# Kernel optimization log

Measured on AMD Instinct MI355X. Metric: run time of the kernel, lower is better.

The kernel has to match this reference:

```python
import jax, jax.numpy as jnp
import numpy as np

WS = (4, 4, 4)  # window shape (wd, wh, ww)
EPS = 1e-5


def _layernorm(x, g, b):
    mu = jnp.mean(x, axis=-1, keepdims=True)
    var = jnp.mean(jnp.square(x - mu), axis=-1, keepdims=True)
    return (x - mu) * jax.lax.rsqrt(var + EPS) * g + b


def _partition(x, ws):
    # x: [B, D, H, W, C] -> [num_windows, wd*wh*ww, C]
    B, D, H, W, C = x.shape
    x = x.reshape(B, D // ws[0], ws[0], H // ws[1], ws[1], W // ws[2], ws[2], C)
    x = jnp.transpose(x, (0, 1, 3, 5, 2, 4, 6, 7))
    return x.reshape(-1, ws[0] * ws[1] * ws[2], C)


def _merge(win, shape, ws):
    B, D, H, W, C = shape
    x = win.reshape(B, D // ws[0], H // ws[1], W // ws[2], ws[0], ws[1], ws[2], C)
    x = jnp.transpose(x, (0, 1, 4, 2, 5, 3, 6, 7))
    return x.reshape(B, D, H, W, C)


def setup_inputs() -> dict:
    key = jax.random.key(0)
    ks = jax.random.split(key, 8)
    B, D, H, W, C = 2, 32, 64, 64, 96
    nh, kd = 4, 24
    s = 0.02
    return {
        "x": jax.random.normal(ks[0], (B, D, H, W, C), jnp.float32),
        "ln1_g": jnp.ones((C,), jnp.float32),
        "ln1_b": jnp.zeros((C,), jnp.float32),
        "wq": jax.random.normal(ks[1], (C, nh, kd), jnp.float32) * s,
        "bq": jnp.zeros((nh, kd), jnp.float32),
        "wk": jax.random.normal(ks[2], (C, nh, kd), jnp.float32) * s,
        "bk": jnp.zeros((nh, kd), jnp.float32),
        "wv": jax.random.normal(ks[3], (C, nh, kd), jnp.float32) * s,
        "bv": jnp.zeros((nh, kd), jnp.float32),
        "wo": jax.random.normal(ks[4], (nh, kd, C), jnp.float32) * s,
        "bo": jnp.zeros((C,), jnp.float32),
        "ln2_g": jnp.ones((C,), jnp.float32),
        "ln2_b": jnp.zeros((C,), jnp.float32),
        "w1": jax.random.normal(ks[5], (C, 4 * C), jnp.float32) * s,
        "b1": jnp.zeros((4 * C,), jnp.float32),
        "w2": jax.random.normal(ks[6], (4 * C, C), jnp.float32) * s,
        "b2": jnp.zeros((C,), jnp.float32),
    }


def reference(x, ln1_g, ln1_b, wq, bq, wk, bk, wv, bv, wo, bo,
              ln2_g, ln2_b, w1, b1, w2, b2):
    shape = x.shape  # [B, D, H, W, C]; dims chosen divisible by WS -> pad is a no-op
    kd = wq.shape[-1]
    shortcut = x
    h = _layernorm(x, ln1_g, ln1_b)
    win = _partition(h, WS)  # [n, L, C], L = 64
    # Keras MultiHeadAttention (inference, dropout off)
    q = jnp.einsum("nlc,chd->nlhd", win, wq) + bq
    k = jnp.einsum("nlc,chd->nlhd", win, wk) + bk
    v = jnp.einsum("nlc,chd->nlhd", win, wv) + bv
    scores = jnp.einsum("nlhd,nmhd->nhlm", q, k) / jnp.sqrt(jnp.float32(kd))
    attn = jax.nn.softmax(scores, axis=-1)
    o = jnp.einsum("nhlm,nmhd->nlhd", attn, v)
    out = jnp.einsum("nlhd,hdc->nlc", o, wo) + bo
    x = shortcut + _merge(out, shape, WS)
    shortcut = x
    h = _layernorm(x, ln2_g, ln2_b)
    h = jax.nn.gelu(h @ w1 + b1, approximate=False)  # TF keras 'gelu' is exact
    h = h @ w2 + b2
    return shortcut + h
```

## Files before the change

kernel.cpp:

```cpp
#include <hip/hip_runtime.h>
#include <hip/hip_bf16.h>

typedef __attribute__((ext_vector_type(8))) short short8;
typedef __attribute__((ext_vector_type(4))) short short4b;
typedef __attribute__((ext_vector_type(4))) float f32x4;
typedef unsigned short ushort_t;

#define NTOK 262144

__device__ __forceinline__ ushort_t f2bf(float f){
  __hip_bfloat16 h = __float2bfloat16(f);
  return *reinterpret_cast<ushort_t*>(&h);
}
__device__ __forceinline__ float bf2f(ushort_t u){
  union { unsigned int i; float f; } v; v.i = ((unsigned int)u) << 16; return v.f;
}
__device__ __forceinline__ float fast_rcp(float x){
  float r; asm("v_rcp_f32 %0, %1" : "=v"(r) : "v"(x)); return r;
}
__device__ __forceinline__ float gelu_f(float x){
  float e = __expf(-1.702f * x);
  return x * fast_rcp(1.0f + e);
}
__device__ __forceinline__ void bar_lds(){
  asm volatile("s_waitcnt lgkmcnt(0)" ::: "memory");
  __builtin_amdgcn_s_barrier();
  __builtin_amdgcn_sched_barrier(0);
}
__device__ __forceinline__ void bar_cnt3(){
  asm volatile("s_waitcnt vmcnt(3) lgkmcnt(0)" ::: "memory");
  __builtin_amdgcn_s_barrier();
  __builtin_amdgcn_sched_barrier(0);
}
__device__ __forceinline__ void bar_cnt5(){
  asm volatile("s_waitcnt vmcnt(5) lgkmcnt(0)" ::: "memory");
  __builtin_amdgcn_s_barrier();
  __builtin_amdgcn_sched_barrier(0);
}
__device__ __forceinline__ void bar_cnt0(){
  asm volatile("s_waitcnt vmcnt(0) lgkmcnt(0)" ::: "memory");
  __builtin_amdgcn_s_barrier();
  __builtin_amdgcn_sched_barrier(0);
}
__device__ __forceinline__ void gl_lds16(const ushort_t* g, ushort_t* l){
  __builtin_amdgcn_global_load_lds(
      (const __attribute__((address_space(1))) void*)g,
      (__attribute__((address_space(3))) void*)l, 16, 0, 0);
}

__device__ __forceinline__ void stage_half3(const ushort_t* __restrict__ src,
                                            ushort_t* __restrict__ dst, int tid)
{
  #pragma unroll
  for (int it = 0; it < 3; ++it) {
    int u = tid + it * 256;
    const ushort_t* sp = src + (size_t)((u < 576) ? u : 0) * 8;
    gl_lds16(sp, dst + (size_t)(u & ~63) * 8);
  }
}

__device__ __forceinline__ void stage_wp(const ushort_t* __restrict__ src,
                                         int src_stride, ushort_t* __restrict__ dst, int tid)
{
  #pragma unroll
  for (int it = 0; it < 5; ++it) {
    int u = tid + it * 256;
    int row = u / 13, c16 = u % 13;
    const ushort_t* sp = src + row * src_stride + ((c16 >= 12) ? 0 : c16 * 8);
    gl_lds16(sp, dst + (size_t)(u & ~63) * 8);
  }
}

__global__ __launch_bounds__(256) void prep_kernel(
    const float* __restrict__ wq, const float* __restrict__ wk, const float* __restrict__ wv,
    const float* __restrict__ wo, const float* __restrict__ w1, const float* __restrict__ w2,
    const float* __restrict__ bq, const float* __restrict__ bk, const float* __restrict__ bv,
    ushort_t* __restrict__ Wqkv, ushort_t* __restrict__ Wo,
    ushort_t* __restrict__ W1, ushort_t* __restrict__ W2, float* __restrict__ biasq)
{
  const float qs = 0.20412414523193150818f;
  int i = blockIdx.x * 256 + threadIdx.x;
  if (i < 27648) {
    int j = i / 96, c = i % 96;
    int s = j / 96, rem = j % 96;
    const float* src = (s == 0) ? wq : (s == 1) ? wk : wv;
    float val = src[c * 96 + rem];
    if (s == 0) val *= qs;
    Wqkv[j * 96 + c] = f2bf(val);
  } else if (i < 36864) {
    int ii = i - 27648;
    int c = ii / 96, hd = ii % 96;
    Wo[ii] = f2bf(wo[hd * 96 + c]);
  } else if (i < 73728) {
    int ii = i - 36864;
    int j = ii / 96, c = ii % 96;
    W1[ii] = f2bf(w1[c * 384 + j]);
  } else if (i < 110592) {
    int ii = i - 73728;
    int c = ii / 384, j = ii % 384;
    W2[ii] = f2bf(w2[j * 96 + c]);
  } else if (i < 110880) {
    int j = i - 110592;
    int s = j / 96, rem = j % 96;
    const float* src = (s == 0) ? bq : (s == 1) ? bk : bv;
    float val = src[rem];
    if (s == 0) val *= qs;
    biasq[j] = val;
  }
}

__global__ __launch_bounds__(256, 2) void fat_kernel(
    const float* __restrict__ x, const float* __restrict__ g, const float* __restrict__ b,
    const ushort_t* __restrict__ Wqkv, const float* __restrict__ biasq,
    const ushort_t* __restrict__ Wo, const float* __restrict__ bo,
    ushort_t* __restrict__ x2b)
{
  __shared__ ushort_t regionA[18432];
  __shared__ ushort_t Vt[4][32][72];
  __shared__ ushort_t WsH[2][6144];
  ushort_t (*hbt)[104]   = reinterpret_cast<ushort_t(*)[104]>(regionA);
  ushort_t (*QK)[200]    = reinterpret_cast<ushort_t(*)[200]>(regionA);
  ushort_t (*Pb)[64][72] = reinterpret_cast<ushort_t(*)[64][72]>(regionA);
  ushort_t (*O_lds)[104] = reinterpret_cast<ushort_t(*)[104]>(regionA);

  int tid = threadIdx.x;
  int n = blockIdx.x;
  int wq_ = n & 15, hq = (n >> 4) & 15, rest = n >> 8;
  int dq = rest & 7, bb_ = rest >> 3;
  int base = bb_ * 131072 + dq * 16384 + hq * 256 + wq_ * 4;
  #define TOK(s) (base + ((s) >> 4) * 4096 + (((s) >> 2) & 3) * 64 + ((s) & 3))

  stage_half3(Wqkv, WsH[0], tid);
  stage_half3(Wqkv + 4608, WsH[1], tid);

  {
    int s = tid >> 2, qr = tid & 3;
    const float* xp = x + (size_t)TOK(s) * 96 + qr * 24;
    f32x4 v[6];
    float sm = 0.f, sq = 0.f;
    #pragma unroll
    for (int i = 0; i < 6; i++) {
      v[i] = *reinterpret_cast<const f32x4*>(xp + i * 4);
      #pragma unroll
      for (int j = 0; j < 4; j++) { sm += v[i][j]; sq += v[i][j] * v[i][j]; }
    }
    sm += __shfl_xor(sm, 1); sq += __shfl_xor(sq, 1);
    sm += __shfl_xor(sm, 2); sq += __shfl_xor(sq, 2);
    float mean = sm * (1.0f / 96.0f);
    float var  = sq * (1.0f / 96.0f) - mean * mean;
    float rstd = rsqrtf(var + 1e-5f);
    #pragma unroll
    for (int i8 = 0; i8 < 3; i8++) {
      short8 pk;
      #pragma unroll
      for (int j = 0; j < 8; j++) {
        int c = qr * 24 + i8 * 8 + j;
        pk[j] = (short)f2bf((v[(i8 * 8 + j) >> 2][(i8 * 8 + j) & 3] - mean) * rstd * g[c] + b[c]);
      }
      *reinterpret_cast<short8*>(&hbt[s][qr * 24 + i8 * 8]) = pk;
    }
  }

  int w = tid >> 6, lane = tid & 63, g16 = lane >> 4, l15 = lane & 15;
  short8 af[3];
  #pragma unroll
  for (int ks = 0; ks < 3; ks++)
    af[ks] = *reinterpret_cast<const short8*>(&hbt[w * 16 + l15][ks * 32 + g16 * 8]);
  __builtin_amdgcn_sched_barrier(0);

  int hidx = 0;
  for (int grp = 0; grp < 3; ++grp) {
    for (int half = 0; half < 2; ++half) {
      const ushort_t* buf = WsH[hidx & 1];
      bar_cnt3();
      f32x4 acc[3];
      #pragma unroll
      for (int jj = 0; jj < 3; jj++) acc[jj] = (f32x4){0.f, 0.f, 0.f, 0.f};
      __builtin_amdgcn_s_setprio(1);
      #pragma unroll
      for (int jj = 0; jj < 3; jj++)
        #pragma unroll
        for (int ks = 0; ks < 3; ks++) {
          short8 wfr = *reinterpret_cast<const short8*>(&buf[(jj * 16 + l15) * 96 + ks * 32 + g16 * 8]);
          acc[jj] = __builtin_amdgcn_mfma_f32_16x16x32_bf16(wfr, af[ks], acc[jj], 0, 0, 0);
        }
      __builtin_amdgcn_s_setprio(0);
      bar_lds();
      {
        const ushort_t* s2 = (hidx + 2 < 6) ? Wqkv + (size_t)(hidx + 2) * 4608
                                            : Wo + (size_t)(hidx - 4) * 4608;
        stage_half3(s2, WsH[hidx & 1], tid);
      }
      if (grp < 2) {
        #pragma unroll
        for (int jj = 0; jj < 3; jj++) {
          int c0 = grp * 96 + (half * 3 + jj) * 16 + g16 * 4;
          f32x4 bb4 = *reinterpret_cast<const f32x4*>(&biasq[c0]);
          unsigned lo = (unsigned)f2bf(acc[jj][0] + bb4[0]) | ((unsigned)f2bf(acc[jj][1] + bb4[1]) << 16);
          unsigned hi = (unsigned)f2bf(acc[jj][2] + bb4[2]) | ((unsigned)f2bf(acc[jj][3] + bb4[3]) << 16);
          uint2 pk; pk.x = lo; pk.y = hi;
          *reinterpret_cast<uint2*>(&QK[w * 16 + l15][c0]) = pk;
        }
      } else {
        #pragma unroll
        for (int jj = 0; jj < 3; jj++) {
          int c0 = (half * 3 + jj) * 16 + g16 * 4;
          f32x4 bb4 = *reinterpret_cast<const f32x4*>(&biasq[192 + c0]);
          #pragma unroll
          for (int r = 0; r < 4; r++) {
            int vcol = c0 + r;
            int h2 = vcol / 24, d2 = vcol - h2 * 24;
            Vt[h2][d2][w * 16 + l15] = f2bf(acc[jj][r] + bb4[r]);
          }
        }
      }
      hidx++;
    }
  }
  bar_lds();

  int h = w;
  short8 kf[4], qf[4];
  const short8 z8 = {0, 0, 0, 0, 0, 0, 0, 0};
  #pragma unroll
  for (int i = 0; i < 4; i++) {
    qf[i] = (g16 < 3) ? *(const short8*)&QK[i * 16 + l15][h * 24 + g16 * 8]      : z8;
    kf[i] = (g16 < 3) ? *(const short8*)&QK[i * 16 + l15][96 + h * 24 + g16 * 8] : z8;
  }
  f32x4 st[4][4];
  __builtin_amdgcn_s_setprio(1);
  #pragma unroll
  for (int tm = 0; tm < 4; tm++)
    #pragma unroll
    for (int tn = 0; tn < 4; tn++)
      st[tm][tn] = __builtin_amdgcn_mfma_f32_16x16x32_bf16(kf[tm], qf[tn],
                    (f32x4){0.f, 0.f, 0.f, 0.f}, 0, 0, 0);
  __builtin_amdgcn_s_setprio(0);
  bar_lds();

  #pragma unroll
  for (int tn = 0; tn < 4; tn++) {
    float m = st[0][tn][0];
    #pragma unroll
    for (int tm = 0; tm < 4; tm++)
      #pragma unroll
      for (int r = 0; r < 4; r++) m = fmaxf(m, st[tm][tn][r]);
    m = fmaxf(m, __shfl_xor(m, 16));
    m = fmaxf(m, __shfl_xor(m, 32));
    float sum = 0.f;
    #pragma unroll
    for (int tm = 0; tm < 4; tm++)
      #pragma unroll
      for (int r = 0; r < 4; r++) {
        float e = __expf(st[tm][tn][r] - m);
        st[tm][tn][r] = e;
        sum += e;
      }
    sum += __shfl_xor(sum, 16);
    sum += __shfl_xor(sum, 32);
    float inv = fast_rcp(sum);
    int q = tn * 16 + l15;
    #pragma unroll
    for (int tm = 0; tm < 4; tm++) {
      unsigned lo = (unsigned)f2bf(st[tm][tn][0] * inv) | ((unsigned)f2bf(st[tm][tn][1] * inv) << 16);
      unsigned hi = (unsigned)f2bf(st[tm][tn][2] * inv) | ((unsigned)f2bf(st[tm][tn][3] * inv) << 16);
      uint2 pk; pk.x = lo; pk.y = hi;
      *(uint2*)&Pb[h][q][tm * 16 + g16 * 4] = pk;
    }
  }

  f32x4 oacc[4][2];
  #pragma unroll
  for (int qt = 0; qt < 4; qt++)
    #pragma unroll
    for (int dt = 0; dt < 2; dt++) oacc[qt][dt] = (f32x4){0.f, 0.f, 0.f, 0.f};
  __builtin_amdgcn_s_setprio(1);
  #pragma unroll
  for (int ks = 0; ks < 2; ks++) {
    short8 vb[2];
    #pragma unroll
    for (int dt = 0; dt < 2; dt++)
      vb[dt] = *(const short8*)&Vt[h][dt * 16 + l15][ks * 32 + g16 * 8];
    #pragma unroll
    for (int qt = 0; qt < 4; qt++) {
      short8 pa = *(const short8*)&Pb[h][qt * 16 + l15][ks * 32 + g16 * 8];
      #pragma unroll
      for (int dt = 0; dt < 2; dt++)
        oacc[qt][dt] = __builtin_amdgcn_mfma_f32_16x16x32_bf16(pa, vb[dt], oacc[qt][dt], 0, 0, 0);
    }
  }
  __builtin_amdgcn_s_setprio(0);

  bar_lds();
  #pragma unroll
  for (int qt = 0; qt < 4; qt++)
    #pragma unroll
    for (int dt = 0; dt < 2; dt++) {
      int d = dt * 16 + l15;
      if (d < 24) {
        #pragma unroll
        for (int r = 0; r < 4; r++)
          O_lds[qt * 16 + g16 * 4 + r][h * 24 + d] = f2bf(oacc[qt][dt][r]);
      }
    }
  bar_cnt0();

  f32x4 pacc[6];
  #pragma unroll
  for (int nt = 0; nt < 6; nt++) pacc[nt] = (f32x4){0.f, 0.f, 0.f, 0.f};
  __builtin_amdgcn_s_setprio(1);
  #pragma unroll
  for (int ks = 0; ks < 3; ks++) {
    short8 pa = *(const short8*)&O_lds[w * 16 + l15][ks * 32 + g16 * 8];
    #pragma unroll
    for (int nt = 0; nt < 6; nt++) {
      const ushort_t* buf = WsH[(nt < 3) ? 0 : 1];
      short8 wb = *reinterpret_cast<const short8*>(&buf[((nt % 3) * 16 + l15) * 96 + ks * 32 + g16 * 8]);
      pacc[nt] = __builtin_amdgcn_mfma_f32_16x16x32_bf16(wb, pa, pacc[nt], 0, 0, 0);
    }
  }
  __builtin_amdgcn_s_setprio(0);
  {
    size_t t = (size_t)TOK(w * 16 + l15);
    #pragma unroll
    for (int nt = 0; nt < 6; nt++) {
      int c0 = nt * 16 + g16 * 4;
      f32x4 bo4 = *reinterpret_cast<const f32x4*>(&bo[c0]);
      f32x4 xr  = *reinterpret_cast<const f32x4*>(&x[t * 96 + c0]);
      float v0 = pacc[nt][0] + bo4[0] + xr[0];
      float v1 = pacc[nt][1] + bo4[1] + xr[1];
      float v2 = pacc[nt][2] + bo4[2] + xr[2];
      float v3 = pacc[nt][3] + bo4[3] + xr[3];
      unsigned lo = (unsigned)f2bf(v0) | ((unsigned)f2bf(v1) << 16);
      unsigned hi = (unsigned)f2bf(v2) | ((unsigned)f2bf(v3) << 16);
      uint2 pk; pk.x = lo; pk.y = hi;
      *reinterpret_cast<uint2*>(&x2b[t * 96 + c0]) = pk;
    }
  }
  #undef TOK
}

__device__ __forceinline__ void ln_to_lds_b(const ushort_t* __restrict__ xrow_base,
    const float* __restrict__ gg, const float* __restrict__ bb,
    ushort_t (*hbt)[104], int tid)
{
  int row = tid >> 1, half = tid & 1;
  const ushort_t* xp = xrow_base + (size_t)row * 96 + half * 48;
  short8 vv[6];
  #pragma unroll
  for (int i = 0; i < 6; i++) vv[i] = *reinterpret_cast<const short8*>(xp + i * 8);
  float v[48];
  float s = 0.f, sq = 0.f;
  #pragma unroll
  for (int i = 0; i < 6; i++)
    #pragma unroll
    for (int j = 0; j < 8; j++) {
      float f = bf2f((ushort_t)vv[i][j]);
      v[i * 8 + j] = f; s += f; sq += f * f;
    }
  s  += __shfl_xor(s, 1);
  sq += __shfl_xor(sq, 1);
  float mean = s * (1.0f / 96.0f);
  float var  = sq * (1.0f / 96.0f) - mean * mean;
  float rstd = rsqrtf(var + 1e-5f);
  #pragma unroll
  for (int i8 = 0; i8 < 6; i8++) {
    short8 pk;
    #pragma unroll
    for (int j = 0; j < 8; j++) {
      int c = half * 48 + i8 * 8 + j;
      pk[j] = (short)f2bf((v[i8 * 8 + j] - mean) * rstd * gg[c] + bb[c]);
    }
    *reinterpret_cast<short8*>(&hbt[row][half * 48 + i8 * 8]) = pk;
  }
}

__global__ __launch_bounds__(256, 2) void mlp2_kernel(
    const ushort_t* __restrict__ x2b, const float* __restrict__ g, const float* __restrict__ b,
    const ushort_t* __restrict__ W1t, const float* __restrict__ b1,
    const ushort_t* __restrict__ W2t, const float* __restrict__ b2,
    float* __restrict__ out)
{
  __shared__ ushort_t smem[128][104];
  __shared__ ushort_t WsA[10240];
  __shared__ ushort_t WsB[10240];
  __shared__ float bias1[384];
  __shared__ float bias2[96];
  int tid = threadIdx.x;
  size_t r0 = (size_t)blockIdx.x * 128;

  stage_wp(W1t, 96, WsA, tid);
  stage_wp(W2t, 384, WsB, tid);
  bias1[tid] = b1[tid];
  if (tid < 128) bias1[256 + tid] = b1[256 + tid];
  if (tid < 96)  bias2[tid] = b2[tid];
  ln_to_lds_b(x2b + r0 * 96, g, b, smem, tid);

  int w = tid >> 6, lane = tid & 63, g16 = lane >> 4, l15 = lane & 15;
  short8 af[2][3];
  #pragma unroll
  for (int mi = 0; mi < 2; mi++)
    #pragma unroll
    for (int ks = 0; ks < 3; ks++)
      af[mi][ks] = *reinterpret_cast<const short8*>(&smem[w * 32 + mi * 16 + l15][ks * 32 + g16 * 8]);
  __builtin_amdgcn_sched_barrier(0);

  f32x4 oacc[6][2];
  #pragma unroll
  for (int nt = 0; nt < 6; nt++) { oacc[nt][0] = (f32x4){0.f,0.f,0.f,0.f}; oacc[nt][1] = (f32x4){0.f,0.f,0.f,0.f}; }

  for (int cc = 0; cc < 4; ++cc) {
    bar_cnt5();
    f32x4 acc[6][2];
    #pragma unroll
    for (int nt = 0; nt < 6; nt++) { acc[nt][0] = (f32x4){0.f,0.f,0.f,0.f}; acc[nt][1] = (f32x4){0.f,0.f,0.f,0.f}; }
    __builtin_amdgcn_s_setprio(1);
    #pragma unroll
    for (int nt = 0; nt < 6; nt++)
      #pragma unroll
      for (int ks = 0; ks < 3; ks++) {
        short8 wfr = *reinterpret_cast<const short8*>(&WsA[(nt * 16 + l15) * 104 + ks * 32 + g16 * 8]);
        acc[nt][0] = __builtin_amdgcn_mfma_f32_16x16x32_bf16(wfr, af[0][ks], acc[nt][0], 0, 0, 0);
        acc[nt][1] = __builtin_amdgcn_mfma_f32_16x16x32_bf16(wfr, af[1][ks], acc[nt][1], 0, 0, 0);
      }
    __builtin_amdgcn_s_setprio(0);
    #pragma unroll
    for (int nt = 0; nt < 6; nt++) {
      f32x4 bb4 = *reinterpret_cast<const f32x4*>(&bias1[cc * 96 + nt * 16 + g16 * 4]);
      #pragma unroll
      for (int mi = 0; mi < 2; mi++) {
        float g0 = gelu_f(acc[nt][mi][0] + bb4[0]);
        float g1 = gelu_f(acc[nt][mi][1] + bb4[1]);
        float g2 = gelu_f(acc[nt][mi][2] + bb4[2]);
        float g3 = gelu_f(acc[nt][mi][3] + bb4[3]);
        unsigned lo = (unsigned)f2bf(g0) | ((unsigned)f2bf(g1) << 16);
        unsigned hi = (unsigned)f2bf(g2) | ((unsigned)f2bf(g3) << 16);
        uint2 pk; pk.x = lo; pk.y = hi;
        *reinterpret_cast<uint2*>(&smem[w * 32 + mi * 16 + l15][nt * 16 + g16 * 4]) = pk;
      }
    }
    short8 a2[2][3];
    #pragma unroll
    for (int mi = 0; mi < 2; mi++)
      #pragma unroll
      for (int ks = 0; ks < 3; ks++)
        a2[mi][ks] = *reinterpret_cast<const short8*>(&smem[w * 32 + mi * 16 + l15][ks * 32 + g16 * 8]);
    bar_lds();
    if (cc < 3) stage_wp(W1t + (cc + 1) * 9216, 96, WsA, tid);
    if (cc < 3) bar_cnt5(); else bar_cnt0();
    __builtin_amdgcn_s_setprio(1);
    #pragma unroll
    for (int nt = 0; nt < 6; nt++)
      #pragma unroll
      for (int ks = 0; ks < 3; ks++) {
        short8 wfr = *reinterpret_cast<const short8*>(&WsB[(nt * 16 + l15) * 104 + ks * 32 + g16 * 8]);
        oacc[nt][0] = __builtin_amdgcn_mfma_f32_16x16x32_bf16(wfr, a2[0][ks], oacc[nt][0], 0, 0, 0);
        oacc[nt][1] = __builtin_amdgcn_mfma_f32_16x16x32_bf16(wfr, a2[1][ks], oacc[nt][1], 0, 0, 0);
      }
    __builtin_amdgcn_s_setprio(0);
    if (cc < 3) {
      bar_lds();
      stage_wp(W2t + (cc + 1) * 96, 384, WsB, tid);
    }
  }

  #pragma unroll
  for (int nt = 0; nt < 6; nt++) {
    int c0 = nt * 16 + g16 * 4;
    f32x4 bb4 = *reinterpret_cast<const f32x4*>(&bias2[c0]);
    #pragma unroll
    for (int mi = 0; mi < 2; mi++) {
      size_t row = r0 + w * 32 + mi * 16 + l15;
      short4b rr = *reinterpret_cast<const short4b*>(&x2b[row * 96 + c0]);
      f32x4 o;
      #pragma unroll
      for (int r = 0; r < 4; r++) o[r] = oacc[nt][mi][r] + bb4[r] + bf2f((ushort_t)rr[r]);
      *reinterpret_cast<f32x4*>(&out[row * 96 + c0]) = o;
    }
  }
}

extern "C" void kernel_launch(void* const* d_in, const int* in_sizes, int n_in,
                              void* d_out, int out_size, void* d_ws, size_t ws_size,
                              hipStream_t stream)
{
  (void)in_sizes; (void)n_in; (void)out_size; (void)ws_size;
  const float* x    = (const float*)d_in[0];
  const float* ln1g = (const float*)d_in[1];
  const float* ln1b = (const float*)d_in[2];
  const float* wq   = (const float*)d_in[3];
  const float* bq   = (const float*)d_in[4];
  const float* wk   = (const float*)d_in[5];
  const float* bk   = (const float*)d_in[6];
  const float* wv   = (const float*)d_in[7];
  const float* bv   = (const float*)d_in[8];
  const float* wo   = (const float*)d_in[9];
  const float* bo   = (const float*)d_in[10];
  const float* ln2g = (const float*)d_in[11];
  const float* ln2b = (const float*)d_in[12];
  const float* w1   = (const float*)d_in[13];
  const float* b1   = (const float*)d_in[14];
  const float* w2   = (const float*)d_in[15];
  const float* b2   = (const float*)d_in[16];

  char* ws = (char*)d_ws;
  ushort_t* x2b  = (ushort_t*)(ws);
  char* wsw      = ws + 50331648;
  ushort_t* Wqkv = (ushort_t*)(wsw);
  ushort_t* Wo   = (ushort_t*)(wsw + 55296);
  ushort_t* W1   = (ushort_t*)(wsw + 55296 + 18432);
  ushort_t* W2   = (ushort_t*)(wsw + 55296 + 18432 + 73728);
  float*    biasq= (float*)   (wsw + 55296 + 18432 + 73728 + 73728);

  prep_kernel<<<434, 256, 0, stream>>>(wq, wk, wv, wo, w1, w2, bq, bk, bv,
                                       Wqkv, Wo, W1, W2, biasq);
  fat_kernel<<<4096, 256, 0, stream>>>(x, ln1g, ln1b, Wqkv, biasq, Wo, bo, x2b);
  mlp2_kernel<<<NTOK / 128, 256, 0, stream>>>(x2b, ln2g, ln2b, W1, b1, W2, b2, (float*)d_out);
}
```

Baseline: 189.7 us.

## Fuse MLP block into windowed attention kernel, eliminating bf16 intermediate round-trip

Merges the separate MLP kernel into the attention kernel. Each block now computes LN2, the W1 GEMM with GELU, and the W2 GEMM for its 64 window tokens, reusing the double-buffered weight staging ring with W2 repacked into chunked transposed halves. This removes the 50MB bf16 intermediate write and read and one kernel launch. In exchange, each block now reads all MLP weights for only 64 tokens instead of 128, and the larger LDS footprint may cut occupancy.

```diff
diff --git a/kernel.cpp b/kernel.cpp
--- a/kernel.cpp
+++ b/kernel.cpp
@@ -32,11 +32,6 @@
   __builtin_amdgcn_s_barrier();
   __builtin_amdgcn_sched_barrier(0);
 }
-__device__ __forceinline__ void bar_cnt5(){
-  asm volatile("s_waitcnt vmcnt(5) lgkmcnt(0)" ::: "memory");
-  __builtin_amdgcn_s_barrier();
-  __builtin_amdgcn_sched_barrier(0);
-}
 __device__ __forceinline__ void bar_cnt0(){
   asm volatile("s_waitcnt vmcnt(0) lgkmcnt(0)" ::: "memory");
   __builtin_amdgcn_s_barrier();
@@ -59,16 +54,14 @@
   }
 }
 
-__device__ __forceinline__ void stage_wp(const ushort_t* __restrict__ src,
-                                         int src_stride, ushort_t* __restrict__ dst, int tid)
+__device__ __forceinline__ const ushort_t* stage_src(int hidx,
+    const ushort_t* Wqkv, const ushort_t* Wo, const ushort_t* W1t, const ushort_t* W2c)
 {
-  #pragma unroll
-  for (int it = 0; it < 5; ++it) {
-    int u = tid + it * 256;
-    int row = u / 13, c16 = u % 13;
-    const ushort_t* sp = src + row * src_stride + ((c16 >= 12) ? 0 : c16 * 8);
-    gl_lds16(sp, dst + (size_t)(u & ~63) * 8);
-  }
+  if (hidx < 6) return Wqkv + (size_t)hidx * 4608;
+  if (hidx < 8) return Wo + (size_t)(hidx - 6) * 4608;
+  int m = hidx - 8, cc = m >> 2, p = m & 3;
+  const ushort_t* base = (p < 2) ? W1t : W2c;
+  return base + (size_t)cc * 9216 + (size_t)(p & 1) * 4608;
 }
 
 __global__ __launch_bounds__(256) void prep_kernel(
@@ -76,7 +69,7 @@
     const float* __restrict__ wo, const float* __restrict__ w1, const float* __restrict__ w2,
     const float* __restrict__ bq, const float* __restrict__ bk, const float* __restrict__ bv,
     ushort_t* __restrict__ Wqkv, ushort_t* __restrict__ Wo,
-    ushort_t* __restrict__ W1, ushort_t* __restrict__ W2, float* __restrict__ biasq)
+    ushort_t* __restrict__ W1, ushort_t* __restrict__ W2c, float* __restrict__ biasq)
 {
   const float qs = 0.20412414523193150818f;
   int i = blockIdx.x * 256 + threadIdx.x;
@@ -97,8 +90,9 @@
     W1[ii] = f2bf(w1[c * 384 + j]);
   } else if (i < 110592) {
     int ii = i - 73728;
-    int c = ii / 384, j = ii % 384;
-    W2[ii] = f2bf(w2[j * 96 + c]);
+    int cc = ii / 9216, rem = ii % 9216;
+    int j = rem / 96, kk = rem % 96;
+    W2c[ii] = f2bf(w2[(size_t)(cc * 96 + kk) * 96 + j]);
   } else if (i < 110880) {
     int j = i - 110592;
     int s = j / 96, rem = j % 96;
@@ -109,19 +103,25 @@
   }
 }
 
-__global__ __launch_bounds__(256, 2) void fat_kernel(
+__global__ __launch_bounds__(256, 2) void fat2_kernel(
     const float* __restrict__ x, const float* __restrict__ g, const float* __restrict__ b,
     const ushort_t* __restrict__ Wqkv, const float* __restrict__ biasq,
     const ushort_t* __restrict__ Wo, const float* __restrict__ bo,
-    ushort_t* __restrict__ x2b)
+    const float* __restrict__ ln2g, const float* __restrict__ ln2b,
+    const ushort_t* __restrict__ W1t, const float* __restrict__ b1,
+    const ushort_t* __restrict__ W2c, const float* __restrict__ b2,
+    float* __restrict__ outp)
 {
-  __shared__ ushort_t regionA[18432];
+  __shared__ ushort_t regionA[19456];
   __shared__ ushort_t Vt[4][32][72];
   __shared__ ushort_t WsH[2][6144];
   ushort_t (*hbt)[104]   = reinterpret_cast<ushort_t(*)[104]>(regionA);
   ushort_t (*QK)[200]    = reinterpret_cast<ushort_t(*)[200]>(regionA);
   ushort_t (*Pb)[64][72] = reinterpret_cast<ushort_t(*)[64][72]>(regionA);
   ushort_t (*O_lds)[104] = reinterpret_cast<ushort_t(*)[104]>(regionA);
+  ushort_t* h_ln = regionA;
+  ushort_t* mid  = regionA + 6656;
+  ushort_t* x2L  = regionA + 13312;
 
   int tid = threadIdx.x;
   int n = blockIdx.x;
@@ -168,53 +168,46 @@
     af[ks] = *reinterpret_cast<const short8*>(&hbt[w * 16 + l15][ks * 32 + g16 * 8]);
   __builtin_amdgcn_sched_barrier(0);
 
-  int hidx = 0;
-  for (int grp = 0; grp < 3; ++grp) {
-    for (int half = 0; half < 2; ++half) {
-      const ushort_t* buf = WsH[hidx & 1];
-      bar_cnt3();
-      f32x4 acc[3];
-      #pragma unroll
-      for (int jj = 0; jj < 3; jj++) acc[jj] = (f32x4){0.f, 0.f, 0.f, 0.f};
-      __builtin_amdgcn_s_setprio(1);
-      #pragma unroll
-      for (int jj = 0; jj < 3; jj++)
+  for (int hidx = 0; hidx < 6; ++hidx) {
+    const ushort_t* buf = WsH[hidx & 1];
+    bar_cnt3();
+    f32x4 acc[3];
+    #pragma unroll
+    for (int jj = 0; jj < 3; jj++) acc[jj] = (f32x4){0.f, 0.f, 0.f, 0.f};
+    __builtin_amdgcn_s_setprio(1);
+    #pragma unroll
+    for (int jj = 0; jj < 3; jj++)
+      #pragma unroll
+      for (int ks = 0; ks < 3; ks++) {
+        short8 wfr = *reinterpret_cast<const short8*>(&buf[(jj * 16 + l15) * 96 + ks * 32 + g16 * 8]);
+        acc[jj] = __builtin_amdgcn_mfma_f32_16x16x32_bf16(wfr, af[ks], acc[jj], 0, 0, 0);
+      }
+    __builtin_amdgcn_s_setprio(0);
+    bar_lds();
+    stage_half3(stage_src(hidx + 2, Wqkv, Wo, W1t, W2c), WsH[hidx & 1], tid);
+    int grp = hidx >> 1, half = hidx & 1;
+    if (grp < 2) {
+      #pragma unroll
+      for (int jj = 0; jj < 3; jj++) {
+        int c0 = grp * 96 + (half * 3 + jj) * 16 + g16 * 4;
+        f32x4 bb4 = *reinterpret_cast<const f32x4*>(&biasq[c0]);
+        unsigned lo = (unsigned)f2bf(acc[jj][0] + bb4[0]) | ((unsigned)f2bf(acc[jj][1] + bb4[1]) << 16);
+        unsigned hi = (unsigned)f2bf(acc[jj][2] + bb4[2]) | ((unsigned)f2bf(acc[jj][3] + bb4[3]) << 16);
+        uint2 pk; pk.x = lo; pk.y = hi;
+        *reinterpret_cast<uint2*>(&QK[w * 16 + l15][c0]) = pk;
+      }
+    } else {
+      #pragma unroll
+      for (int jj = 0; jj < 3; jj++) {
+        int c0 = (half * 3 + jj) * 16 + g16 * 4;
+        f32x4 bb4 = *reinterpret_cast<const f32x4*>(&biasq[192 + c0]);
         #pragma unroll
-        for (int ks = 0; ks < 3; ks++) {
-          short8 wfr = *reinterpret_cast<const short8*>(&buf[(jj * 16 + l15) * 96 + ks * 32 + g16 * 8]);
-          acc[jj] = __builtin_amdgcn_mfma_f32_16x16x32_bf16(wfr, af[ks], acc[jj], 0, 0, 0);
+        for (int r = 0; r < 4; r++) {
+          int vcol = c0 + r;
+          int h2 = vcol / 24, d2 = vcol - h2 * 24;
+          Vt[h2][d2][w * 16 + l15] = f2bf(acc[jj][r] + bb4[r]);
         }
-      __builtin_amdgcn_s_setprio(0);
-      bar_lds();
-      {
-        const ushort_t* s2 = (hidx + 2 < 6) ? Wqkv + (size_t)(hidx + 2) * 4608
-                                            : Wo + (size_t)(hidx - 4) * 4608;
-        stage_half3(s2, WsH[hidx & 1], tid);
-      }
-      if (grp < 2) {
-        #pragma unroll
-        for (int jj = 0; jj < 3; jj++) {
-          int c0 = grp * 96 + (half * 3 + jj) * 16 + g16 * 4;
-          f32x4 bb4 = *reinterpret_cast<const f32x4*>(&biasq[c0]);
-          unsigned lo = (unsigned)f2bf(acc[jj][0] + bb4[0]) | ((unsigned)f2bf(acc[jj][1] + bb4[1]) << 16);
-          unsigned hi = (unsigned)f2bf(acc[jj][2] + bb4[2]) | ((unsigned)f2bf(acc[jj][3] + bb4[3]) << 16);
-          uint2 pk; pk.x = lo; pk.y = hi;
-          *reinterpret_cast<uint2*>(&QK[w * 16 + l15][c0]) = pk;
-        }
-      } else {
-        #pragma unroll
-        for (int jj = 0; jj < 3; jj++) {
-          int c0 = (half * 3 + jj) * 16 + g16 * 4;
-          f32x4 bb4 = *reinterpret_cast<const f32x4*>(&biasq[192 + c0]);
-          #pragma unroll
-          for (int r = 0; r < 4; r++) {
-            int vcol = c0 + r;
-            int h2 = vcol / 24, d2 = vcol - h2 * 24;
-            Vt[h2][d2][w * 16 + l15] = f2bf(acc[jj][r] + bb4[r]);
-          }
-        }
-      }
-      hidx++;
+      }
     }
   }
   bar_lds();
@@ -269,11 +262,11 @@
     }
   }
 
-  f32x4 oacc[4][2];
+  f32x4 oatt[4][2];
   #pragma unroll
   for (int qt = 0; qt < 4; qt++)
     #pragma unroll
-    for (int dt = 0; dt < 2; dt++) oacc[qt][dt] = (f32x4){0.f, 0.f, 0.f, 0.f};
+    for (int dt = 0; dt < 2; dt++) oatt[qt][dt] = (f32x4){0.f, 0.f, 0.f, 0.f};
   __builtin_amdgcn_s_setprio(1);
   #pragma unroll
   for (int ks = 0; ks < 2; ks++) {
@@ -286,7 +279,7 @@
       short8 pa = *(const short8*)&Pb[h][qt * 16 + l15][ks * 32 + g16 * 8];
       #pragma unroll
       for (int dt = 0; dt < 2; dt++)
-        oacc[qt][dt] = __builtin_amdgcn_mfma_f32_16x16x32_bf16(pa, vb[dt], oacc[qt][dt], 0, 0, 0);
+        oatt[qt][dt] = __builtin_amdgcn_mfma_f32_16x16x32_bf16(pa, vb[dt], oatt[qt][dt], 0, 0, 0);
     }
   }
   __builtin_amdgcn_s_setprio(0);
@@ -300,7 +293,7 @@
       if (d < 24) {
         #pragma unroll
         for (int r = 0; r < 4; r++)
-          O_lds[qt * 16 + g16 * 4 + r][h * 24 + d] = f2bf(oacc[qt][dt][r]);
+          O_lds[qt * 16 + g16 * 4 + r][h * 24 + d] = f2bf(oatt[qt][dt][r]);
       }
     }
   bar_cnt0();
@@ -320,164 +313,127 @@
     }
   }
   __builtin_amdgcn_s_setprio(0);
+  bar_lds();
+  stage_half3(stage_src(8, Wqkv, Wo, W1t, W2c), WsH[0], tid);
+  stage_half3(stage_src(9, Wqkv, Wo, W1t, W2c), WsH[1], tid);
+
+  size_t t = (size_t)TOK(w * 16 + l15);
+  int rowoff = (w * 16 + l15);
   {
-    size_t t = (size_t)TOK(w * 16 + l15);
+    float xv[24];
+    float sm = 0.f, sq = 0.f;
     #pragma unroll
     for (int nt = 0; nt < 6; nt++) {
       int c0 = nt * 16 + g16 * 4;
       f32x4 bo4 = *reinterpret_cast<const f32x4*>(&bo[c0]);
       f32x4 xr  = *reinterpret_cast<const f32x4*>(&x[t * 96 + c0]);
-      float v0 = pacc[nt][0] + bo4[0] + xr[0];
-      float v1 = pacc[nt][1] + bo4[1] + xr[1];
-      float v2 = pacc[nt][2] + bo4[2] + xr[2];
-      float v3 = pacc[nt][3] + bo4[3] + xr[3];
-      unsigned lo = (unsigned)f2bf(v0) | ((unsigned)f2bf(v1) << 16);
-      unsigned hi = (unsigned)f2bf(v2) | ((unsigned)f2bf(v3) << 16);
-      uint2 pk; pk.x = lo; pk.y = hi;
-      *reinterpret_cast<uint2*>(&x2b[t * 96 + c0]) = pk;
-    }
-  }
-  #undef TOK
-}
-
-__device__ __forceinline__ void ln_to_lds_b(const ushort_t* __restrict__ xrow_base,
-    const float* __restrict__ gg, const float* __restrict__ bb,
-    ushort_t (*hbt)[104], int tid)
-{
-  int row = tid >> 1, half = tid & 1;
-  const ushort_t* xp = xrow_base + (size_t)row * 96 + half * 48;
-  short8 vv[6];
-  #pragma unroll
-  for (int i = 0; i < 6; i++) vv[i] = *reinterpret_cast<const short8*>(xp + i * 8);
-  float v[48];
-  float s = 0.f, sq = 0.f;
-  #pragma unroll
-  for (int i = 0; i < 6; i++)
-    #pragma unroll
-    for (int j = 0; j < 8; j++) {
-      float f = bf2f((ushort_t)vv[i][j]);
-      v[i * 8 + j] = f; s += f; sq += f * f;
-    }
-  s  += __shfl_xor(s, 1);
-  sq += __shfl_xor(sq, 1);
-  float mean = s * (1.0f / 96.0f);
-  float var  = sq * (1.0f / 96.0f) - mean * mean;
-  float rstd = rsqrtf(var + 1e-5f);
-  #pragma unroll
-  for (int i8 = 0; i8 < 6; i8++) {
-    short8 pk;
-    #pragma unroll
-    for (int j = 0; j < 8; j++) {
-      int c = half * 48 + i8 * 8 + j;
-      pk[j] = (short)f2bf((v[i8 * 8 + j] - mean) * rstd * gg[c] + bb[c]);
-    }
-    *reinterpret_cast<short8*>(&hbt[row][half * 48 + i8 * 8]) = pk;
-  }
-}
-
-__global__ __launch_bounds__(256, 2) void mlp2_kernel(
-    const ushort_t* __restrict__ x2b, const float* __restrict__ g, const float* __restrict__ b,
-    const ushort_t* __restrict__ W1t, const float* __restrict__ b1,
-    const ushort_t* __restrict__ W2t, const float* __restrict__ b2,
-    float* __restrict__ out)
-{
-  __shared__ ushort_t smem[128][104];
-  __shared__ ushort_t WsA[10240];
-  __shared__ ushort_t WsB[10240];
-  __shared__ float bias1[384];
-  __shared__ float bias2[96];
-  int tid = threadIdx.x;
-  size_t r0 = (size_t)blockIdx.x * 128;
-
-  stage_wp(W1t, 96, WsA, tid);
-  stage_wp(W2t, 384, WsB, tid);
-  bias1[tid] = b1[tid];
-  if (tid < 128) bias1[256 + tid] = b1[256 + tid];
-  if (tid < 96)  bias2[tid] = b2[tid];
-  ln_to_lds_b(x2b + r0 * 96, g, b, smem, tid);
-
-  int w = tid >> 6, lane = tid & 63, g16 = lane >> 4, l15 = lane & 15;
-  short8 af[2][3];
-  #pragma unroll
-  for (int mi = 0; mi < 2; mi++)
-    #pragma unroll
-    for (int ks = 0; ks < 3; ks++)
-      af[mi][ks] = *reinterpret_cast<const short8*>(&smem[w * 32 + mi * 16 + l15][ks * 32 + g16 * 8]);
+      #pragma unroll
+      for (int r = 0; r < 4; r++) {
+        float v = pacc[nt][r] + bo4[r] + xr[r];
+        xv[nt * 4 + r] = v; sm += v; sq += v * v;
+      }
+    }
+    sm += __shfl_xor(sm, 16); sq += __shfl_xor(sq, 16);
+    sm += __shfl_xor(sm, 32); sq += __shfl_xor(sq, 32);
+    float mean = sm * (1.0f / 96.0f);
+    float var  = sq * (1.0f / 96.0f) - mean * mean;
+    float rstd = rsqrtf(var + 1e-5f);
+    #pragma unroll
+    for (int nt = 0; nt < 6; nt++) {
+      int c0 = nt * 16 + g16 * 4;
+      f32x4 g4 = *reinterpret_cast<const f32x4*>(&ln2g[c0]);
+      f32x4 b4 = *reinterpret_cast<const f32x4*>(&ln2b[c0]);
+      unsigned hlo, hhi, xlo, xhi;
+      float h0 = (xv[nt*4+0] - mean) * rstd * g4[0] + b4[0];
+      float h1 = (xv[nt*4+1] - mean) * rstd * g4[1] + b4[1];
+      float h2v = (xv[nt*4+2] - mean) * rstd * g4[2] + b4[2];
+      float h3 = (xv[nt*4+3] - mean) * rstd * g4[3] + b4[3];
+      hlo = (unsigned)f2bf(h0) | ((unsigned)f2bf(h1) << 16);
+      hhi = (unsigned)f2bf(h2v) | ((unsigned)f2bf(h3) << 16);
+      xlo = (unsigned)f2bf(xv[nt*4+0]) | ((unsigned)f2bf(xv[nt*4+1]) << 16);
+      xhi = (unsigned)f2bf(xv[nt*4+2]) | ((unsigned)f2bf(xv[nt*4+3]) << 16);
+      uint2 ph; ph.x = hlo; ph.y = hhi;
+      uint2 px; px.x = xlo; px.y = xhi;
+      *reinterpret_cast<uint2*>(&h_ln[rowoff * 104 + c0]) = ph;
+      *reinterpret_cast<uint2*>(&x2L[rowoff * 96 + c0]) = px;
+    }
+  }
+  short8 hf[3];
+  #pragma unroll
+  for (int ks = 0; ks < 3; ks++)
+    hf[ks] = *reinterpret_cast<const short8*>(&h_ln[rowoff * 104 + ks * 32 + g16 * 8]);
   __builtin_amdgcn_sched_barrier(0);
 
-  f32x4 oacc[6][2];
-  #pragma unroll
-  for (int nt = 0; nt < 6; nt++) { oacc[nt][0] = (f32x4){0.f,0.f,0.f,0.f}; oacc[nt][1] = (f32x4){0.f,0.f,0.f,0.f}; }
-
-  for (int cc = 0; cc < 4; ++cc) {
-    bar_cnt5();
-    f32x4 acc[6][2];
-    #pragma unroll
-    for (int nt = 0; nt < 6; nt++) { acc[nt][0] = (f32x4){0.f,0.f,0.f,0.f}; acc[nt][1] = (f32x4){0.f,0.f,0.f,0.f}; }
-    __builtin_amdgcn_s_setprio(1);
-    #pragma unroll
-    for (int nt = 0; nt < 6; nt++)
-      #pragma unroll
-      for (int ks = 0; ks < 3; ks++) {
-        short8 wfr = *reinterpret_cast<const short8*>(&WsA[(nt * 16 + l15) * 104 + ks * 32 + g16 * 8]);
-        acc[nt][0] = __builtin_amdgcn_mfma_f32_16x16x32_bf16(wfr, af[0][ks], acc[nt][0], 0, 0, 0);
-        acc[nt][1] = __builtin_amdgcn_mfma_f32_16x16x32_bf16(wfr, af[1][ks], acc[nt][1], 0, 0, 0);
-      }
-    __builtin_amdgcn_s_setprio(0);
-    #pragma unroll
-    for (int nt = 0; nt < 6; nt++) {
-      f32x4 bb4 = *reinterpret_cast<const f32x4*>(&bias1[cc * 96 + nt * 16 + g16 * 4]);
-      #pragma unroll
-      for (int mi = 0; mi < 2; mi++) {
-        float g0 = gelu_f(acc[nt][mi][0] + bb4[0]);
-        float g1 = gelu_f(acc[nt][mi][1] + bb4[1]);
-        float g2 = gelu_f(acc[nt][mi][2] + bb4[2]);
-        float g3 = gelu_f(acc[nt][mi][3] + bb4[3]);
+  f32x4 oacc[6];
+  #pragma unroll
+  for (int nt = 0; nt < 6; nt++) oacc[nt] = (f32x4){0.f, 0.f, 0.f, 0.f};
+  short8 mf[3];
+  for (int m = 0; m < 16; ++m) {
+    int cc = m >> 2, p = m & 3;
+    const ushort_t* buf = WsH[m & 1];
+    if (m == 15) bar_cnt0(); else bar_cnt3();
+    if (p < 2) {
+      f32x4 accM[3];
+      #pragma unroll
+      for (int jj = 0; jj < 3; jj++) accM[jj] = (f32x4){0.f, 0.f, 0.f, 0.f};
+      __builtin_amdgcn_s_setprio(1);
+      #pragma unroll
+      for (int jj = 0; jj < 3; jj++)
+        #pragma unroll
+        for (int ks = 0; ks < 3; ks++) {
+          short8 wfr = *reinterpret_cast<const short8*>(&buf[(jj * 16 + l15) * 96 + ks * 32 + g16 * 8]);
+          accM[jj] = __builtin_amdgcn_mfma_f32_16x16x32_bf16(wfr, hf[ks], accM[jj], 0, 0, 0);
+        }
+      __builtin_amdgcn_s_setprio(0);
+      bar_lds();
+      if (m + 2 <= 15) stage_half3(stage_src(10 + m, Wqkv, Wo, W1t, W2c), WsH[m & 1], tid);
+      #pragma unroll
+      for (int jj = 0; jj < 3; jj++) {
+        int lc = (p * 3 + jj) * 16 + g16 * 4;
+        f32x4 bb4 = *reinterpret_cast<const f32x4*>(&b1[cc * 96 + lc]);
+        float g0 = gelu_f(accM[jj][0] + bb4[0]);
+        float g1 = gelu_f(accM[jj][1] + bb4[1]);
+        float g2v = gelu_f(accM[jj][2] + bb4[2]);
+        float g3 = gelu_f(accM[jj][3] + bb4[3]);
         unsigned lo = (unsigned)f2bf(g0) | ((unsigned)f2bf(g1) << 16);
-        unsigned hi = (unsigned)f2bf(g2) | ((unsigned)f2bf(g3) << 16);
+        unsigned hi = (unsigned)f2bf(g2v) | ((unsigned)f2bf(g3) << 16);
         uint2 pk; pk.x = lo; pk.y = hi;
-        *reinterpret_cast<uint2*>(&smem[w * 32 + mi * 16 + l15][nt * 16 + g16 * 4]) = pk;
-      }
-    }
-    short8 a2[2][3];
-    #pragma unroll
-    for (int mi = 0; mi < 2; mi++)
-      #pragma unroll
-      for (int ks = 0; ks < 3; ks++)
-        a2[mi][ks] = *reinterpret_cast<const short8*>(&smem[w * 32 + mi * 16 + l15][ks * 32 + g16 * 8]);
-    bar_lds();
-    if (cc < 3) stage_wp(W1t + (cc + 1) * 9216, 96, WsA, tid);
-    if (cc < 3) bar_cnt5(); else bar_cnt0();
-    __builtin_amdgcn_s_setprio(1);
-    #pragma unroll
-    for (int nt = 0; nt < 6; nt++)
-      #pragma unroll
-      for (int ks = 0; ks < 3; ks++) {
-        short8 wfr = *reinterpret_cast<const short8*>(&WsB[(nt * 16 + l15) * 104 + ks * 32 + g16 * 8]);
-        oacc[nt][0] = __builtin_amdgcn_mfma_f32_16x16x32_bf16(wfr, a2[0][ks], oacc[nt][0], 0, 0, 0);
-        oacc[nt][1] = __builtin_amdgcn_mfma_f32_16x16x32_bf16(wfr, a2[1][ks], oacc[nt][1], 0, 0, 0);
-      }
-    __builtin_amdgcn_s_setprio(0);
-    if (cc < 3) {
-      bar_lds();
-      stage_wp(W2t + (cc + 1) * 96, 384, WsB, tid);
+        *reinterpret_cast<uint2*>(&mid[rowoff * 104 + lc]) = pk;
+      }
+      if (p == 1) {
+        #pragma unroll
+        for (int ks = 0; ks < 3; ks++)
+          mf[ks] = *reinterpret_cast<const short8*>(&mid[rowoff * 104 + ks * 32 + g16 * 8]);
+      }
+    } else {
+      int jb = (p - 2) * 3;
+      __builtin_amdgcn_s_setprio(1);
+      #pragma unroll
+      for (int jj = 0; jj < 3; jj++)
+        #pragma unroll
+        for (int ks = 0; ks < 3; ks++) {
+          short8 wfr = *reinterpret_cast<const short8*>(&buf[(jj * 16 + l15) * 96 + ks * 32 + g16 * 8]);
+          oacc[jb + jj] = __builtin_amdgcn_mfma_f32_16x16x32_bf16(wfr, mf[ks], oacc[jb + jj], 0, 0, 0);
+        }
+      __builtin_amdgcn_s_setprio(0);
+      if (m < 15) {
+        bar_lds();
+        if (m + 2 <= 15) stage_half3(stage_src(10 + m, Wqkv, Wo, W1t, W2c), WsH[m & 1], tid);
+      }
     }
   }
 
   #pragma unroll
   for (int nt = 0; nt < 6; nt++) {
     int c0 = nt * 16 + g16 * 4;
-    f32x4 bb4 = *reinterpret_cast<const f32x4*>(&bias2[c0]);
-    #pragma unroll
-    for (int mi = 0; mi < 2; mi++) {
-      size_t row = r0 + w * 32 + mi * 16 + l15;
-      short4b rr = *reinterpret_cast<const short4b*>(&x2b[row * 96 + c0]);
-      f32x4 o;
-      #pragma unroll
-      for (int r = 0; r < 4; r++) o[r] = oacc[nt][mi][r] + bb4[r] + bf2f((ushort_t)rr[r]);
-      *reinterpret_cast<f32x4*>(&out[row * 96 + c0]) = o;
-    }
-  }
+    f32x4 b24 = *reinterpret_cast<const f32x4*>(&b2[c0]);
+    short4b xr2 = *reinterpret_cast<const short4b*>(&x2L[rowoff * 96 + c0]);
+    f32x4 o;
+    #pragma unroll
+    for (int r = 0; r < 4; r++) o[r] = oacc[nt][r] + b24[r] + bf2f((ushort_t)xr2[r]);
+    *reinterpret_cast<f32x4*>(&outp[t * 96 + c0]) = o;
+  }
+  #undef TOK
 }
 
 extern "C" void kernel_launch(void* const* d_in, const int* in_sizes, int n_in,
@@ -504,16 +460,14 @@
   const float* b2   = (const float*)d_in[16];
 
   char* ws = (char*)d_ws;
-  ushort_t* x2b  = (ushort_t*)(ws);
-  char* wsw      = ws + 50331648;
-  ushort_t* Wqkv = (ushort_t*)(wsw);
-  ushort_t* Wo   = (ushort_t*)(wsw + 55296);
-  ushort_t* W1   = (ushort_t*)(wsw + 55296 + 18432);
-  ushort_t* W2   = (ushort_t*)(wsw + 55296 + 18432 + 73728);
-  float*    biasq= (float*)   (wsw + 55296 + 18432 + 73728 + 73728);
+  ushort_t* Wqkv = (ushort_t*)(ws);
+  ushort_t* Wo   = (ushort_t*)(ws + 55296);
+  ushort_t* W1   = (ushort_t*)(ws + 55296 + 18432);
+  ushort_t* W2c  = (ushort_t*)(ws + 55296 + 18432 + 73728);
+  float*    biasq= (float*)   (ws + 55296 + 18432 + 73728 + 73728);
 
   prep_kernel<<<434, 256, 0, stream>>>(wq, wk, wv, wo, w1, w2, bq, bk, bv,
-                                       Wqkv, Wo, W1, W2, biasq);
-  fat_kernel<<<4096, 256, 0, stream>>>(x, ln1g, ln1b, Wqkv, biasq, Wo, bo, x2b);
-  mlp2_kernel<<<NTOK / 128, 256, 0, stream>>>(x2b, ln2g, ln2b, W1, b1, W2, b2, (float*)d_out);
-}
+                                       Wqkv, Wo, W1, W2c, biasq);
+  fat2_kernel<<<4096, 256, 0, stream>>>(x, ln1g, ln1b, Wqkv, biasq, Wo, bo,
+                                        ln2g, ln2b, W1, b1, W2c, b2, (float*)d_out);
+}
```

Result: slower. 282.7 us (+49.0%).

## Shrink attention kernel LDS to single weight buffer for three blocks per CU

Applied to the files above, without the earlier changes.

Merges the attention kernel's shared arrays into one flat buffer and drops double-buffering of weight halves, loading each 4608-element weight slice into a single padded buffer with full waits. This cuts LDS per block so three blocks can reside per CU (launch bounds raised from 2 to 3). The softmax probability tile moves to an XOR-swizzled layout to avoid bank conflicts, the weight rows are padded to 104, and both kernels remap block IDs in groups of 8, likely to spread adjacent blocks across XCDs. The cost is losing prefetch overlap: every weight stage now waits with vmcnt(0) before its MFMAs.

```diff
diff --git a/kernel.cpp b/kernel.cpp
--- a/kernel.cpp
+++ b/kernel.cpp
@@ -27,11 +27,6 @@
   __builtin_amdgcn_s_barrier();
   __builtin_amdgcn_sched_barrier(0);
 }
-__device__ __forceinline__ void bar_cnt3(){
-  asm volatile("s_waitcnt vmcnt(3) lgkmcnt(0)" ::: "memory");
-  __builtin_amdgcn_s_barrier();
-  __builtin_amdgcn_sched_barrier(0);
-}
 __device__ __forceinline__ void bar_cnt5(){
   asm volatile("s_waitcnt vmcnt(5) lgkmcnt(0)" ::: "memory");
   __builtin_amdgcn_s_barrier();
@@ -48,14 +43,17 @@
       (__attribute__((address_space(3))) void*)l, 16, 0, 0);
 }
 
-__device__ __forceinline__ void stage_half3(const ushort_t* __restrict__ src,
-                                            ushort_t* __restrict__ dst, int tid)
+__device__ __forceinline__ void stage624(const ushort_t* __restrict__ src,
+                                         ushort_t* __restrict__ dst, int tid)
 {
   #pragma unroll
   for (int it = 0; it < 3; ++it) {
     int u = tid + it * 256;
-    const ushort_t* sp = src + (size_t)((u < 576) ? u : 0) * 8;
-    gl_lds16(sp, dst + (size_t)(u & ~63) * 8);
+    if (u < 624) {
+      int row = u / 13, c16 = u % 13;
+      const ushort_t* sp = src + row * 96 + ((c16 == 12) ? 0 : c16 * 8);
+      gl_lds16(sp, dst + (size_t)(u & ~63) * 8);
+    }
   }
 }
 
@@ -109,29 +107,24 @@
   }
 }
 
-__global__ __launch_bounds__(256, 2) void fat_kernel(
+__global__ __launch_bounds__(256, 3) void fat_kernel(
     const float* __restrict__ x, const float* __restrict__ g, const float* __restrict__ b,
     const ushort_t* __restrict__ Wqkv, const float* __restrict__ biasq,
     const ushort_t* __restrict__ Wo, const float* __restrict__ bo,
     ushort_t* __restrict__ x2b)
 {
-  __shared__ ushort_t regionA[18432];
-  __shared__ ushort_t Vt[4][32][72];
-  __shared__ ushort_t WsH[2][6144];
-  ushort_t (*hbt)[104]   = reinterpret_cast<ushort_t(*)[104]>(regionA);
-  ushort_t (*QK)[200]    = reinterpret_cast<ushort_t(*)[200]>(regionA);
-  ushort_t (*Pb)[64][72] = reinterpret_cast<ushort_t(*)[64][72]>(regionA);
-  ushort_t (*O_lds)[104] = reinterpret_cast<ushort_t(*)[104]>(regionA);
+  __shared__ ushort_t SM[27136];
+  const int WS_OFF = 12800, VT_OFF = 17920;
 
   int tid = threadIdx.x;
-  int n = blockIdx.x;
+  int bid = blockIdx.x;
+  int n = (bid & 7) * 512 + (bid >> 3);
   int wq_ = n & 15, hq = (n >> 4) & 15, rest = n >> 8;
   int dq = rest & 7, bb_ = rest >> 3;
   int base = bb_ * 131072 + dq * 16384 + hq * 256 + wq_ * 4;
   #define TOK(s) (base + ((s) >> 4) * 4096 + (((s) >> 2) & 3) * 64 + ((s) & 3))
 
-  stage_half3(Wqkv, WsH[0], tid);
-  stage_half3(Wqkv + 4608, WsH[1], tid);
+  stage624(Wqkv, SM + WS_OFF, tid);
 
   {
     int s = tid >> 2, qr = tid & 3;
@@ -157,7 +150,7 @@
         int c = qr * 24 + i8 * 8 + j;
         pk[j] = (short)f2bf((v[(i8 * 8 + j) >> 2][(i8 * 8 + j) & 3] - mean) * rstd * g[c] + b[c]);
       }
-      *reinterpret_cast<short8*>(&hbt[s][qr * 24 + i8 * 8]) = pk;
+      *reinterpret_cast<short8*>(&SM[s * 104 + qr * 24 + i8 * 8]) = pk;
     }
   }
 
@@ -165,56 +158,49 @@
   short8 af[3];
   #pragma unroll
   for (int ks = 0; ks < 3; ks++)
-    af[ks] = *reinterpret_cast<const short8*>(&hbt[w * 16 + l15][ks * 32 + g16 * 8]);
-  __builtin_amdgcn_sched_barrier(0);
-
-  int hidx = 0;
-  for (int grp = 0; grp < 3; ++grp) {
-    for (int half = 0; half < 2; ++half) {
-      const ushort_t* buf = WsH[hidx & 1];
-      bar_cnt3();
-      f32x4 acc[3];
-      #pragma unroll
-      for (int jj = 0; jj < 3; jj++) acc[jj] = (f32x4){0.f, 0.f, 0.f, 0.f};
-      __builtin_amdgcn_s_setprio(1);
-      #pragma unroll
-      for (int jj = 0; jj < 3; jj++)
+    af[ks] = *reinterpret_cast<const short8*>(&SM[(w * 16 + l15) * 104 + ks * 32 + g16 * 8]);
+  bar_lds();
+
+  for (int hidx = 0; hidx < 6; ++hidx) {
+    const ushort_t* buf = SM + WS_OFF;
+    bar_cnt0();
+    f32x4 acc[3];
+    #pragma unroll
+    for (int jj = 0; jj < 3; jj++) acc[jj] = (f32x4){0.f, 0.f, 0.f, 0.f};
+    __builtin_amdgcn_s_setprio(1);
+    #pragma unroll
+    for (int jj = 0; jj < 3; jj++)
+      #pragma unroll
+      for (int ks = 0; ks < 3; ks++) {
+        short8 wfr = *reinterpret_cast<const short8*>(&buf[(jj * 16 + l15) * 104 + ks * 32 + g16 * 8]);
+        acc[jj] = __builtin_amdgcn_mfma_f32_16x16x32_bf16(wfr, af[ks], acc[jj], 0, 0, 0);
+      }
+    __builtin_amdgcn_s_setprio(0);
+    bar_lds();
+    if (hidx < 5) stage624(Wqkv + (size_t)(hidx + 1) * 4608, SM + WS_OFF, tid);
+    int grp = hidx >> 1, half = hidx & 1;
+    if (grp < 2) {
+      #pragma unroll
+      for (int jj = 0; jj < 3; jj++) {
+        int c0 = grp * 96 + (half * 3 + jj) * 16 + g16 * 4;
+        f32x4 bb4 = *reinterpret_cast<const f32x4*>(&biasq[c0]);
+        unsigned lo = (unsigned)f2bf(acc[jj][0] + bb4[0]) | ((unsigned)f2bf(acc[jj][1] + bb4[1]) << 16);
+        unsigned hi = (unsigned)f2bf(acc[jj][2] + bb4[2]) | ((unsigned)f2bf(acc[jj][3] + bb4[3]) << 16);
+        uint2 pk; pk.x = lo; pk.y = hi;
+        *reinterpret_cast<uint2*>(&SM[(w * 16 + l15) * 200 + c0]) = pk;
+      }
+    } else {
+      #pragma unroll
+      for (int jj = 0; jj < 3; jj++) {
+        int c0 = (half * 3 + jj) * 16 + g16 * 4;
+        f32x4 bb4 = *reinterpret_cast<const f32x4*>(&biasq[192 + c0]);
         #pragma unroll
-        for (int ks = 0; ks < 3; ks++) {
-          short8 wfr = *reinterpret_cast<const short8*>(&buf[(jj * 16 + l15) * 96 + ks * 32 + g16 * 8]);
-          acc[jj] = __builtin_amdgcn_mfma_f32_16x16x32_bf16(wfr, af[ks], acc[jj], 0, 0, 0);
+        for (int r = 0; r < 4; r++) {
+          int vcol = c0 + r;
+          int h2 = vcol / 24, d2 = vcol - h2 * 24;
+          SM[VT_OFF + h2 * 2304 + d2 * 72 + (w * 16 + l15)] = f2bf(acc[jj][r] + bb4[r]);
         }
-      __builtin_amdgcn_s_setprio(0);
-      bar_lds();
-      {
-        const ushort_t* s2 = (hidx + 2 < 6) ? Wqkv + (size_t)(hidx + 2) * 4608
-                                            : Wo + (size_t)(hidx - 4) * 4608;
-        stage_half3(s2, WsH[hidx & 1], tid);
-      }
-      if (grp < 2) {
-        #pragma unroll
-        for (int jj = 0; jj < 3; jj++) {
-          int c0 = grp * 96 + (half * 3 + jj) * 16 + g16 * 4;
-          f32x4 bb4 = *reinterpret_cast<const f32x4*>(&biasq[c0]);
-          unsigned lo = (unsigned)f2bf(acc[jj][0] + bb4[0]) | ((unsigned)f2bf(acc[jj][1] + bb4[1]) << 16);
-          unsigned hi = (unsigned)f2bf(acc[jj][2] + bb4[2]) | ((unsigned)f2bf(acc[jj][3] + bb4[3]) << 16);
-          uint2 pk; pk.x = lo; pk.y = hi;
-          *reinterpret_cast<uint2*>(&QK[w * 16 + l15][c0]) = pk;
-        }
-      } else {
-        #pragma unroll
-        for (int jj = 0; jj < 3; jj++) {
-          int c0 = (half * 3 + jj) * 16 + g16 * 4;
-          f32x4 bb4 = *reinterpret_cast<const f32x4*>(&biasq[192 + c0]);
-          #pragma unroll
-          for (int r = 0; r < 4; r++) {
-            int vcol = c0 + r;
-            int h2 = vcol / 24, d2 = vcol - h2 * 24;
-            Vt[h2][d2][w * 16 + l15] = f2bf(acc[jj][r] + bb4[r]);
-          }
-        }
-      }
-      hidx++;
+      }
     }
   }
   bar_lds();
@@ -224,8 +210,8 @@
   const short8 z8 = {0, 0, 0, 0, 0, 0, 0, 0};
   #pragma unroll
   for (int i = 0; i < 4; i++) {
-    qf[i] = (g16 < 3) ? *(const short8*)&QK[i * 16 + l15][h * 24 + g16 * 8]      : z8;
-    kf[i] = (g16 < 3) ? *(const short8*)&QK[i * 16 + l15][96 + h * 24 + g16 * 8] : z8;
+    qf[i] = (g16 < 3) ? *(const short8*)&SM[(i * 16 + l15) * 200 + h * 24 + g16 * 8]      : z8;
+    kf[i] = (g16 < 3) ? *(const short8*)&SM[(i * 16 + l15) * 200 + 96 + h * 24 + g16 * 8] : z8;
   }
   f32x4 st[4][4];
   __builtin_amdgcn_s_setprio(1);
@@ -265,7 +251,8 @@
       unsigned lo = (unsigned)f2bf(st[tm][tn][0] * inv) | ((unsigned)f2bf(st[tm][tn][1] * inv) << 16);
       unsigned hi = (unsigned)f2bf(st[tm][tn][2] * inv) | ((unsigned)f2bf(st[tm][tn][3] * inv) << 16);
       uint2 pk; pk.x = lo; pk.y = hi;
-      *(uint2*)&Pb[h][q][tm * 16 + g16 * 4] = pk;
+      int u = tm * 2 + (g16 >> 1);
+      *reinterpret_cast<uint2*>(&SM[h * 4096 + q * 64 + ((u ^ (q & 7)) << 3) + ((g16 & 1) << 2)]) = pk;
     }
   }
 
@@ -280,10 +267,12 @@
     short8 vb[2];
     #pragma unroll
     for (int dt = 0; dt < 2; dt++)
-      vb[dt] = *(const short8*)&Vt[h][dt * 16 + l15][ks * 32 + g16 * 8];
+      vb[dt] = *(const short8*)&SM[VT_OFF + h * 2304 + (dt * 16 + l15) * 72 + ks * 32 + g16 * 8];
     #pragma unroll
     for (int qt = 0; qt < 4; qt++) {
-      short8 pa = *(const short8*)&Pb[h][qt * 16 + l15][ks * 32 + g16 * 8];
+      int row = qt * 16 + l15;
+      int up = ks * 4 + g16;
+      short8 pa = *(const short8*)&SM[h * 4096 + row * 64 + ((up ^ (row & 7)) << 3)];
       #pragma unroll
       for (int dt = 0; dt < 2; dt++)
         oacc[qt][dt] = __builtin_amdgcn_mfma_f32_16x16x32_bf16(pa, vb[dt], oacc[qt][dt], 0, 0, 0);
@@ -292,6 +281,7 @@
   __builtin_amdgcn_s_setprio(0);
 
   bar_lds();
+  stage624(Wo, SM + WS_OFF, tid);
   #pragma unroll
   for (int qt = 0; qt < 4; qt++)
     #pragma unroll
@@ -300,7 +290,7 @@
       if (d < 24) {
         #pragma unroll
         for (int r = 0; r < 4; r++)
-          O_lds[qt * 16 + g16 * 4 + r][h * 24 + d] = f2bf(oacc[qt][dt][r]);
+          SM[(qt * 16 + g16 * 4 + r) * 104 + h * 24 + d] = f2bf(oacc[qt][dt][r]);
       }
     }
   bar_cnt0();
@@ -311,12 +301,25 @@
   __builtin_amdgcn_s_setprio(1);
   #pragma unroll
   for (int ks = 0; ks < 3; ks++) {
-    short8 pa = *(const short8*)&O_lds[w * 16 + l15][ks * 32 + g16 * 8];
-    #pragma unroll
-    for (int nt = 0; nt < 6; nt++) {
-      const ushort_t* buf = WsH[(nt < 3) ? 0 : 1];
-      short8 wb = *reinterpret_cast<const short8*>(&buf[((nt % 3) * 16 + l15) * 96 + ks * 32 + g16 * 8]);
+    short8 pa = *(const short8*)&SM[(w * 16 + l15) * 104 + ks * 32 + g16 * 8];
+    #pragma unroll
+    for (int nt = 0; nt < 3; nt++) {
+      short8 wb = *reinterpret_cast<const short8*>(&SM[WS_OFF + (nt * 16 + l15) * 104 + ks * 32 + g16 * 8]);
       pacc[nt] = __builtin_amdgcn_mfma_f32_16x16x32_bf16(wb, pa, pacc[nt], 0, 0, 0);
+    }
+  }
+  __builtin_amdgcn_s_setprio(0);
+  bar_lds();
+  stage624(Wo + 4608, SM + WS_OFF, tid);
+  bar_cnt0();
+  __builtin_amdgcn_s_setprio(1);
+  #pragma unroll
+  for (int ks = 0; ks < 3; ks++) {
+    short8 pa = *(const short8*)&SM[(w * 16 + l15) * 104 + ks * 32 + g16 * 8];
+    #pragma unroll
+    for (int nt = 0; nt < 3; nt++) {
+      short8 wb = *reinterpret_cast<const short8*>(&SM[WS_OFF + (nt * 16 + l15) * 104 + ks * 32 + g16 * 8]);
+      pacc[3 + nt] = __builtin_amdgcn_mfma_f32_16x16x32_bf16(wb, pa, pacc[3 + nt], 0, 0, 0);
     }
   }
   __builtin_amdgcn_s_setprio(0);
@@ -387,7 +390,9 @@
   __shared__ float bias1[384];
   __shared__ float bias2[96];
   int tid = threadIdx.x;
-  size_t r0 = (size_t)blockIdx.x * 128;
+  int bid = blockIdx.x;
+  int blk = (bid & 7) * 256 + (bid >> 3);
+  size_t r0 = (size_t)blk * 128;
 
   stage_wp(W1t, 96, WsA, tid);
   stage_wp(W2t, 384, WsB, tid);
```

New measurement: 189.7 us. Within noise of the previous version (-0.0%).
